# Kernel tuning notes

Measured on AMD Instinct MI355X. Metric: run time of the kernel, lower is better.

Reference implementation:

```python
import jax, jax.numpy as jnp
import numpy as np

MARGIN = 0.2  # init margin
B, D = 4096, 512


def _pairwise_dist(x):
    # torch.cdist(x, x, p=2): Euclidean distance via Gram matrix
    sq = jnp.sum(x * x, axis=-1)                      # [B]
    gram = x @ x.T                                    # [B, B]
    d2 = jnp.maximum(sq[:, None] + sq[None, :] - 2.0 * gram, 0.0)
    safe = jnp.where(d2 > 0, d2, 1.0)                 # grad-safe sqrt at 0
    return jnp.where(d2 > 0, jnp.sqrt(safe), 0.0)


def setup_inputs() -> dict:
    key = jax.random.key(0)
    k1, k2, k3 = jax.random.split(key, 3)
    anchor = jax.random.normal(k1, (B, D), dtype=jnp.float32)
    positive = jax.random.normal(k2, (B, D), dtype=jnp.float32)
    labels = jax.random.randint(k3, (B,), 0, 64)
    return {"anchor": anchor, "positive": positive, "labels": labels}


def reference(anchor, positive, labels):
    d_ap = jnp.sum((anchor - positive) ** 2, axis=-1)          # [B] squared dist
    pd = _pairwise_dist(anchor)                                 # [B, B] euclidean
    diff_label = labels[None, :] != labels[:, None]             # [B, B]
    inf = jnp.float32(jnp.inf)
    # negatives farther than the positive (note: pd is euclidean, d_ap squared,
    # exactly as in the original code)
    cand = jnp.where(diff_label & (pd > d_ap[:, None]), pd, inf)
    min_larger = jnp.min(cand, axis=1)
    # fallback: min over all different-label negatives
    fallback = jnp.min(jnp.where(diff_label, pd, inf), axis=1)
    d_an = jnp.where(jnp.isfinite(min_larger), min_larger, fallback)
    loss = jnp.maximum(d_ap - d_an + MARGIN, 0.0)
    return jnp.mean(loss)
```

## Files before the change

### kernel.cpp

```cpp
#include <hip/hip_runtime.h>
#include <hip/hip_bf16.h>
#include <cstdint>
#include <cstddef>

constexpr int BN = 4096;
constexpr int DN = 512;
constexpr int NT = BN / 128;
constexpr int NBLK = NT * (NT + 1) / 2;
constexpr float MARGIN = 0.2f;
constexpr uint32_t INF_U = 0x7f800000u;

typedef __attribute__((ext_vector_type(8))) short short8;
typedef __attribute__((ext_vector_type(4))) float float4v;

__global__ __launch_bounds__(256) void prep_kernel(
    const float* __restrict__ anchor,
    const float* __restrict__ positive,
    const int* __restrict__ labels,
    uint16_t* __restrict__ Abf,
    float4* __restrict__ meta,
    uint32_t* __restrict__ min_all,
    uint32_t* __restrict__ min_larger,
    uint32_t* __restrict__ done_count)
{
    const int tid  = threadIdx.x;
    const int wave = tid >> 6;
    const int lane = tid & 63;
    const int row  = blockIdx.x * 4 + wave;

    if (blockIdx.x == 0 && tid == 0) *done_count = 0;

    const float4* arow = (const float4*)(anchor   + (size_t)row * DN);
    const float4* prow = (const float4*)(positive + (size_t)row * DN);

    float4 av0 = arow[lane * 2 + 0], av1 = arow[lane * 2 + 1];
    float4 pv0 = prow[lane * 2 + 0], pv1 = prow[lane * 2 + 1];

    float a[8] = {av0.x, av0.y, av0.z, av0.w, av1.x, av1.y, av1.z, av1.w};
    float p[8] = {pv0.x, pv0.y, pv0.z, pv0.w, pv1.x, pv1.y, pv1.z, pv1.w};

    float s = 0.f, d = 0.f;
    union { uint16_t u[8]; uint4 v; } pk;
    #pragma unroll
    for (int i = 0; i < 8; ++i) {
        s += a[i] * a[i];
        float dx = a[i] - p[i];
        d += dx * dx;
        uint32_t ub = __float_as_uint(a[i]);
        pk.u[i] = (uint16_t)((ub + 0x7fffu + ((ub >> 16) & 1u)) >> 16);
    }

    ((uint4*)(Abf + (size_t)row * DN))[lane] = pk.v;

    #pragma unroll
    for (int off = 32; off; off >>= 1) {
        s += __shfl_xor(s, off);
        d += __shfl_xor(d, off);
    }
    if (lane == 0) {
        meta[row] = (float4){s, d, d * d, __uint_as_float((uint32_t)labels[row])};
        min_all[row]    = INF_U;
        min_larger[row] = INF_U;
    }
}

__global__ __launch_bounds__(256, 3) void gram_kernel(
    const uint16_t* __restrict__ Abf,
    const float4* __restrict__ meta,
    uint32_t* __restrict__ min_all,
    uint32_t* __restrict__ min_larger,
    uint32_t* __restrict__ done_count,
    float* __restrict__ out)
{
    __shared__ uint16_t Abuf[128 * 64];
    __shared__ uint16_t Bbuf[128 * 64];

    int t = blockIdx.x, bi = 0, rem = NT;
    while (t >= rem) { t -= rem; ++bi; --rem; }
    const int bj = bi + t;
    const bool offdiag = (bi != bj);
    const int rowBase = bi * 128;
    const int colBase = bj * 128;

    const int tid  = threadIdx.x;
    const int wave = tid >> 6;
    const int lane = tid & 63;
    const int wi   = wave >> 1;
    const int wj   = wave & 1;
    const int quad = lane >> 4;
    const int l15  = lane & 15;

    int sr[4], sc[4], sp[4];
    #pragma unroll
    for (int i = 0; i < 4; ++i) {
        int l = tid + i * 256;
        sr[i] = l >> 3; sc[i] = l & 7; sp[i] = sc[i] ^ (sr[i] & 7);
    }

    float4v acc[4][4];
    #pragma unroll
    for (int i = 0; i < 4; ++i)
        #pragma unroll
        for (int j = 0; j < 4; ++j)
            acc[i][j] = (float4v){0.f, 0.f, 0.f, 0.f};

    for (int kt = 0; kt < DN / 64; ++kt) {
        const int k0 = kt * 64;
        __syncthreads();
        {
            uint4 st[4];
            #pragma unroll
            for (int i = 0; i < 4; ++i)
                st[i] = *(const uint4*)(Abf + (size_t)(rowBase + sr[i]) * DN + k0 + sc[i] * 8);
            #pragma unroll
            for (int i = 0; i < 4; ++i)
                *(uint4*)(Abuf + sr[i] * 64 + sp[i] * 8) = st[i];
            #pragma unroll
            for (int i = 0; i < 4; ++i)
                st[i] = *(const uint4*)(Abf + (size_t)(colBase + sr[i]) * DN + k0 + sc[i] * 8);
            #pragma unroll
            for (int i = 0; i < 4; ++i)
                *(uint4*)(Bbuf + sr[i] * 64 + sp[i] * 8) = st[i];
        }
        __syncthreads();

        #pragma unroll
        for (int kk = 0; kk < 2; ++kk) {
            short8 af[4], bfr[4];
            #pragma unroll
            for (int mi = 0; mi < 4; ++mi) {
                int r = wi * 64 + mi * 16 + l15;
                int p = (kk * 4 + quad) ^ (r & 7);
                af[mi] = *(const short8*)(Abuf + r * 64 + p * 8);
            }
            #pragma unroll
            for (int mj = 0; mj < 4; ++mj) {
                int r = wj * 64 + mj * 16 + l15;
                int p = (kk * 4 + quad) ^ (r & 7);
                bfr[mj] = *(const short8*)(Bbuf + r * 64 + p * 8);
            }
            #pragma unroll
            for (int mi = 0; mi < 4; ++mi)
                #pragma unroll
                for (int mj = 0; mj < 4; ++mj)
                    acc[mi][mj] = __builtin_amdgcn_mfma_f32_16x16x32_bf16(
                        af[mi], bfr[mj], acc[mi][mj], 0, 0, 0);
        }
    }

    const float INFF = __uint_as_float(INF_U);
    float4 mj_meta[4];
    #pragma unroll
    for (int mj = 0; mj < 4; ++mj)
        mj_meta[mj] = meta[colBase + wj * 64 + mj * 16 + l15];

    float cAll[4], cLarger[4];
    #pragma unroll
    for (int mj = 0; mj < 4; ++mj) { cAll[mj] = INFF; cLarger[mj] = INFF; }

    #pragma unroll
    for (int mi = 0; mi < 4; ++mi) {
        #pragma unroll
        for (int r = 0; r < 4; ++r) {
            int row = rowBase + wi * 64 + mi * 16 + quad * 4 + r;
            float4 mim = meta[row];
            uint32_t li = __float_as_uint(mim.w);
            float mAll = INFF, mLarger = INFF;
            #pragma unroll
            for (int mj = 0; mj < 4; ++mj) {
                float d2 = mim.x + mj_meta[mj].x - 2.0f * acc[mi][mj][r];
                d2 = d2 > 0.f ? d2 : 0.f;
                if (__float_as_uint(mj_meta[mj].w) != li) {
                    mAll = fminf(mAll, d2);
                    if (d2 > mim.z) mLarger = fminf(mLarger, d2);
                    if (offdiag) {
                        cAll[mj] = fminf(cAll[mj], d2);
                        if (d2 > mj_meta[mj].z) cLarger[mj] = fminf(cLarger[mj], d2);
                    }
                }
            }
            #pragma unroll
            for (int off = 1; off < 16; off <<= 1) {
                mAll    = fminf(mAll,    __shfl_xor(mAll, off));
                mLarger = fminf(mLarger, __shfl_xor(mLarger, off));
            }
            if (l15 == 0) {
                atomicMin(&min_all[row],    __float_as_uint(mAll));
                atomicMin(&min_larger[row], __float_as_uint(mLarger));
            }
        }
    }
    if (offdiag) {
        #pragma unroll
        for (int mj = 0; mj < 4; ++mj) {
            float a0 = cAll[mj], l0 = cLarger[mj];
            a0 = fminf(a0, __shfl_xor(a0, 16)); l0 = fminf(l0, __shfl_xor(l0, 16));
            a0 = fminf(a0, __shfl_xor(a0, 32)); l0 = fminf(l0, __shfl_xor(l0, 32));
            if (quad == 0) {
                int col = colBase + wj * 64 + mj * 16 + l15;
                atomicMin(&min_all[col],    __float_as_uint(a0));
                atomicMin(&min_larger[col], __float_as_uint(l0));
            }
        }
    }

    __shared__ bool isLast;
    __syncthreads();
    if (tid == 0) {
        __threadfence();
        isLast = (atomicAdd(done_count, 1u) == NBLK - 1);
    }
    __syncthreads();
    if (isLast) {
        __threadfence();
        float s = 0.f;
        for (int i = tid; i < BN; i += 256) {
            uint32_t mlu = __hip_atomic_load(&min_larger[i], __ATOMIC_RELAXED, __HIP_MEMORY_SCOPE_AGENT);
            uint32_t mau = __hip_atomic_load(&min_all[i],    __ATOMIC_RELAXED, __HIP_MEMORY_SCOPE_AGENT);
            float dan2 = (mlu != INF_U) ? __uint_as_float(mlu) : __uint_as_float(mau);
            float l = meta[i].y - sqrtf(dan2) + MARGIN;
            s += l > 0.f ? l : 0.f;
        }
        #pragma unroll
        for (int off = 32; off; off >>= 1) s += __shfl_xor(s, off);
        __shared__ float wsum[4];
        if ((tid & 63) == 0) wsum[tid >> 6] = s;
        __syncthreads();
        if (tid == 0) out[0] = (wsum[0] + wsum[1] + wsum[2] + wsum[3]) * (1.0f / BN);
    }
}

extern "C" void kernel_launch(void* const* d_in, const int* in_sizes, int n_in,
                              void* d_out, int out_size, void* d_ws, size_t ws_size,
                              hipStream_t stream) {
    const float* anchor   = (const float*)d_in[0];
    const float* positive = (const float*)d_in[1];
    const int*   labels   = (const int*)d_in[2];
    float* out = (float*)d_out;

    uint8_t* ws = (uint8_t*)d_ws;
    uint16_t* Abf        = (uint16_t*)ws;
    float4*   meta       = (float4*)(ws + (size_t)BN * DN * 2);
    uint32_t* min_all    = (uint32_t*)(meta + BN);
    uint32_t* min_larger = min_all + BN;
    uint32_t* done_count = min_larger + BN;

    prep_kernel<<<BN / 4, 256, 0, stream>>>(anchor, positive, labels, Abf, meta,
                                            min_all, min_larger, done_count);
    gram_kernel<<<NBLK, 256, 0, stream>>>(Abf, meta, min_all, min_larger, done_count, out);
}
```

Before: 106.1 us.

## Load MFMA operands directly from global memory instead of LDS staging

Removes the shared-memory tiles and barriers from the Gram kernel. Each wave now loads its bf16 MFMA fragments straight from global memory, with the K loop fully unrolled. This drops the LDS round-trip and the __syncthreads, and relies on L1/L2 to serve the data the waves share. The occupancy hint is lowered from 3 to 2 waves per SIMD to give the unrolled loads room in registers, at the cost of more global traffic and less latency hiding.

```diff
diff --git a/kernel.cpp b/kernel.cpp
--- a/kernel.cpp
+++ b/kernel.cpp
@@ -64,7 +64,7 @@
     }
 }
 
-__global__ __launch_bounds__(256, 3) void gram_kernel(
+__global__ __launch_bounds__(256, 2) void gram_kernel(
     const uint16_t* __restrict__ Abf,
     const float4* __restrict__ meta,
     uint32_t* __restrict__ min_all,
@@ -72,9 +72,6 @@
     uint32_t* __restrict__ done_count,
     float* __restrict__ out)
 {
-    __shared__ uint16_t Abuf[128 * 64];
-    __shared__ uint16_t Bbuf[128 * 64];
-
     int t = blockIdx.x, bi = 0, rem = NT;
     while (t >= rem) { t -= rem; ++bi; --rem; }
     const int bj = bi + t;
@@ -90,12 +87,8 @@
     const int quad = lane >> 4;
     const int l15  = lane & 15;
 
-    int sr[4], sc[4], sp[4];
-    #pragma unroll
-    for (int i = 0; i < 4; ++i) {
-        int l = tid + i * 256;
-        sr[i] = l >> 3; sc[i] = l & 7; sp[i] = sc[i] ^ (sr[i] & 7);
-    }
+    const uint16_t* aBase = Abf + (size_t)(rowBase + wi * 64 + l15) * DN + quad * 8;
+    const uint16_t* bBase = Abf + (size_t)(colBase + wj * 64 + l15) * DN + quad * 8;
 
     float4v acc[4][4];
     #pragma unroll
@@ -104,48 +97,21 @@
         for (int j = 0; j < 4; ++j)
             acc[i][j] = (float4v){0.f, 0.f, 0.f, 0.f};
 
-    for (int kt = 0; kt < DN / 64; ++kt) {
-        const int k0 = kt * 64;
-        __syncthreads();
-        {
-            uint4 st[4];
+    #pragma unroll
+    for (int kc = 0; kc < DN / 32; ++kc) {
+        short8 af[4], bfr[4];
+        #pragma unroll
+        for (int mi = 0; mi < 4; ++mi)
+            af[mi] = *(const short8*)(aBase + mi * 16 * DN + kc * 32);
+        #pragma unroll
+        for (int mj = 0; mj < 4; ++mj)
+            bfr[mj] = *(const short8*)(bBase + mj * 16 * DN + kc * 32);
+        #pragma unroll
+        for (int mi = 0; mi < 4; ++mi)
             #pragma unroll
-            for (int i = 0; i < 4; ++i)
-                st[i] = *(const uint4*)(Abf + (size_t)(rowBase + sr[i]) * DN + k0 + sc[i] * 8);
-            #pragma unroll
-            for (int i = 0; i < 4; ++i)
-                *(uint4*)(Abuf + sr[i] * 64 + sp[i] * 8) = st[i];
-            #pragma unroll
-            for (int i = 0; i < 4; ++i)
-                st[i] = *(const uint4*)(Abf + (size_t)(colBase + sr[i]) * DN + k0 + sc[i] * 8);
-            #pragma unroll
-            for (int i = 0; i < 4; ++i)
-                *(uint4*)(Bbuf + sr[i] * 64 + sp[i] * 8) = st[i];
-        }
-        __syncthreads();
-
-        #pragma unroll
-        for (int kk = 0; kk < 2; ++kk) {
-            short8 af[4], bfr[4];
-            #pragma unroll
-            for (int mi = 0; mi < 4; ++mi) {
-                int r = wi * 64 + mi * 16 + l15;
-                int p = (kk * 4 + quad) ^ (r & 7);
-                af[mi] = *(const short8*)(Abuf + r * 64 + p * 8);
-            }
-            #pragma unroll
-            for (int mj = 0; mj < 4; ++mj) {
-                int r = wj * 64 + mj * 16 + l15;
-                int p = (kk * 4 + quad) ^ (r & 7);
-                bfr[mj] = *(const short8*)(Bbuf + r * 64 + p * 8);
-            }
-            #pragma unroll
-            for (int mi = 0; mi < 4; ++mi)
-                #pragma unroll
-                for (int mj = 0; mj < 4; ++mj)
-                    acc[mi][mj] = __builtin_amdgcn_mfma_f32_16x16x32_bf16(
-                        af[mi], bfr[mj], acc[mi][mj], 0, 0, 0);
-        }
+            for (int mj = 0; mj < 4; ++mj)
+                acc[mi][mj] = __builtin_amdgcn_mfma_f32_16x16x32_bf16(
+                    af[mi], bfr[mj], acc[mi][mj], 0, 0, 0);
     }
 
     const float INFF = __uint_as_float(INF_U);
```

Result: slower. 136.4 us (+28.6%).

## Shrink gram tiles to 64x64 and prefetch next K-slice into registers

Applied to the files above, without the earlier changes.

Reduces the symmetric Gram tile from 128x128 to 64x64, which gives many more blocks (2080 instead of 528) and raises the occupancy hint from 3 to 4 blocks per CU. It also adds register double-buffering: the next K-slice is loaded from global memory while the current one is stored to LDS and consumed by MFMA. The goal is better load balancing across CUs and hidden global load latency. The cost is lower arithmetic intensity per tile, more global traffic, and more atomicMin operations in the epilogue.

```diff
diff --git a/kernel.cpp b/kernel.cpp
--- a/kernel.cpp
+++ b/kernel.cpp
@@ -5,7 +5,8 @@
 
 constexpr int BN = 4096;
 constexpr int DN = 512;
-constexpr int NT = BN / 128;
+constexpr int TN = 64;
+constexpr int NT = BN / TN;
 constexpr int NBLK = NT * (NT + 1) / 2;
 constexpr float MARGIN = 0.2f;
 constexpr uint32_t INF_U = 0x7f800000u;
@@ -64,7 +65,7 @@
     }
 }
 
-__global__ __launch_bounds__(256, 3) void gram_kernel(
+__global__ __launch_bounds__(256, 4) void gram_kernel(
     const uint16_t* __restrict__ Abf,
     const float4* __restrict__ meta,
     uint32_t* __restrict__ min_all,
@@ -72,15 +73,15 @@
     uint32_t* __restrict__ done_count,
     float* __restrict__ out)
 {
-    __shared__ uint16_t Abuf[128 * 64];
-    __shared__ uint16_t Bbuf[128 * 64];
+    __shared__ uint16_t Abuf[TN * 64];
+    __shared__ uint16_t Bbuf[TN * 64];
 
     int t = blockIdx.x, bi = 0, rem = NT;
     while (t >= rem) { t -= rem; ++bi; --rem; }
     const int bj = bi + t;
     const bool offdiag = (bi != bj);
-    const int rowBase = bi * 128;
-    const int colBase = bj * 128;
+    const int rowBase = bi * TN;
+    const int colBase = bj * TN;
 
     const int tid  = threadIdx.x;
     const int wave = tid >> 6;
@@ -90,84 +91,92 @@
     const int quad = lane >> 4;
     const int l15  = lane & 15;
 
-    int sr[4], sc[4], sp[4];
-    #pragma unroll
-    for (int i = 0; i < 4; ++i) {
+    int sr[2], sc[2], sp[2];
+    #pragma unroll
+    for (int i = 0; i < 2; ++i) {
         int l = tid + i * 256;
         sr[i] = l >> 3; sc[i] = l & 7; sp[i] = sc[i] ^ (sr[i] & 7);
     }
 
-    float4v acc[4][4];
-    #pragma unroll
-    for (int i = 0; i < 4; ++i)
-        #pragma unroll
-        for (int j = 0; j < 4; ++j)
+    float4v acc[2][2];
+    #pragma unroll
+    for (int i = 0; i < 2; ++i)
+        #pragma unroll
+        for (int j = 0; j < 2; ++j)
             acc[i][j] = (float4v){0.f, 0.f, 0.f, 0.f};
 
+    uint4 stA[2], stB[2];
+    #pragma unroll
+    for (int i = 0; i < 2; ++i) {
+        stA[i] = *(const uint4*)(Abf + (size_t)(rowBase + sr[i]) * DN + sc[i] * 8);
+        stB[i] = *(const uint4*)(Abf + (size_t)(colBase + sr[i]) * DN + sc[i] * 8);
+    }
+
+    #pragma unroll
     for (int kt = 0; kt < DN / 64; ++kt) {
-        const int k0 = kt * 64;
         __syncthreads();
-        {
-            uint4 st[4];
-            #pragma unroll
-            for (int i = 0; i < 4; ++i)
-                st[i] = *(const uint4*)(Abf + (size_t)(rowBase + sr[i]) * DN + k0 + sc[i] * 8);
-            #pragma unroll
-            for (int i = 0; i < 4; ++i)
-                *(uint4*)(Abuf + sr[i] * 64 + sp[i] * 8) = st[i];
-            #pragma unroll
-            for (int i = 0; i < 4; ++i)
-                st[i] = *(const uint4*)(Abf + (size_t)(colBase + sr[i]) * DN + k0 + sc[i] * 8);
-            #pragma unroll
-            for (int i = 0; i < 4; ++i)
-                *(uint4*)(Bbuf + sr[i] * 64 + sp[i] * 8) = st[i];
+        uint4 nA[2], nB[2];
+        if (kt < DN / 64 - 1) {
+            const int k0 = (kt + 1) * 64;
+            #pragma unroll
+            for (int i = 0; i < 2; ++i) {
+                nA[i] = *(const uint4*)(Abf + (size_t)(rowBase + sr[i]) * DN + k0 + sc[i] * 8);
+                nB[i] = *(const uint4*)(Abf + (size_t)(colBase + sr[i]) * DN + k0 + sc[i] * 8);
+            }
+        }
+        #pragma unroll
+        for (int i = 0; i < 2; ++i) {
+            *(uint4*)(Abuf + sr[i] * 64 + sp[i] * 8) = stA[i];
+            *(uint4*)(Bbuf + sr[i] * 64 + sp[i] * 8) = stB[i];
         }
         __syncthreads();
 
         #pragma unroll
         for (int kk = 0; kk < 2; ++kk) {
-            short8 af[4], bfr[4];
-            #pragma unroll
-            for (int mi = 0; mi < 4; ++mi) {
-                int r = wi * 64 + mi * 16 + l15;
+            short8 af[2], bfr[2];
+            #pragma unroll
+            for (int mi = 0; mi < 2; ++mi) {
+                int r = wi * 32 + mi * 16 + l15;
                 int p = (kk * 4 + quad) ^ (r & 7);
                 af[mi] = *(const short8*)(Abuf + r * 64 + p * 8);
             }
             #pragma unroll
-            for (int mj = 0; mj < 4; ++mj) {
-                int r = wj * 64 + mj * 16 + l15;
+            for (int mj = 0; mj < 2; ++mj) {
+                int r = wj * 32 + mj * 16 + l15;
                 int p = (kk * 4 + quad) ^ (r & 7);
                 bfr[mj] = *(const short8*)(Bbuf + r * 64 + p * 8);
             }
             #pragma unroll
-            for (int mi = 0; mi < 4; ++mi)
+            for (int mi = 0; mi < 2; ++mi)
                 #pragma unroll
-                for (int mj = 0; mj < 4; ++mj)
+                for (int mj = 0; mj < 2; ++mj)
                     acc[mi][mj] = __builtin_amdgcn_mfma_f32_16x16x32_bf16(
                         af[mi], bfr[mj], acc[mi][mj], 0, 0, 0);
         }
+        #pragma unroll
+        for (int i = 0; i < 2; ++i) { stA[i] = nA[i]; stB[i] = nB[i]; }
     }
 
     const float INFF = __uint_as_float(INF_U);
-    float4 mj_meta[4];
-    #pragma unroll
-    for (int mj = 0; mj < 4; ++mj)
-        mj_meta[mj] = meta[colBase + wj * 64 + mj * 16 + l15];
-
-    float cAll[4], cLarger[4];
-    #pragma unroll
-    for (int mj = 0; mj < 4; ++mj) { cAll[mj] = INFF; cLarger[mj] = INFF; }
-
-    #pragma unroll
-    for (int mi = 0; mi < 4; ++mi) {
+    float4 mj_meta[2];
+    #pragma unroll
+    for (int mj = 0; mj < 2; ++mj)
+        mj_meta[mj] = meta[colBase + wj * 32 + mj * 16 + l15];
+
+    float cAll[2], cLarger[2];
+    #pragma unroll
+    for (int mj = 0; mj < 2; ++mj) { cAll[mj] = INFF; cLarger[mj] = INFF; }
+
+    #pragma unroll
+    for (int mi = 0; mi < 2; ++mi) {
         #pragma unroll
         for (int r = 0; r < 4; ++r) {
-            int row = rowBase + wi * 64 + mi * 16 + quad * 4 + r;
+            int row = rowBase + wi * 32 + mi * 16 + quad * 4 + r;
             float4 mim = meta[row];
             uint32_t li = __float_as_uint(mim.w);
             float mAll = INFF, mLarger = INFF;
             #pragma unroll
-            for (int mj = 0; mj < 4; ++mj) {
+            for (int mj = 0; mj < 2; ++mj) {
                 float d2 = mim.x + mj_meta[mj].x - 2.0f * acc[mi][mj][r];
                 d2 = d2 > 0.f ? d2 : 0.f;
                 if (__float_as_uint(mj_meta[mj].w) != li) {
@@ -192,12 +201,12 @@
     }
     if (offdiag) {
         #pragma unroll
-        for (int mj = 0; mj < 4; ++mj) {
+        for (int mj = 0; mj < 2; ++mj) {
             float a0 = cAll[mj], l0 = cLarger[mj];
             a0 = fminf(a0, __shfl_xor(a0, 16)); l0 = fminf(l0, __shfl_xor(l0, 16));
             a0 = fminf(a0, __shfl_xor(a0, 32)); l0 = fminf(l0, __shfl_xor(l0, 32));
             if (quad == 0) {
-                int col = colBase + wj * 64 + mj * 16 + l15;
+                int col = colBase + wj * 32 + mj * 16 + l15;
                 atomicMin(&min_all[col],    __float_as_uint(a0));
                 atomicMin(&min_larger[col], __float_as_uint(l0));
             }
```

New measurement: 309.2 us. 2.91x slower.
